# Kernel optimization log

Hardware: AMD Instinct MI355X
Metric: run time of the kernel (lower is better)

Reference implementation:

```python
import jax, jax.numpy as jnp
import numpy as np

NUM_CLASSES = 80
NUM_PRIORS = 3
STRIDES = (8, 16, 32)
ANCHORS = (((10, 13), (16, 30), (33, 23)),
           ((30, 61), (62, 45), (59, 119)),
           ((116, 90), (156, 198), (373, 326)))
PRE_TOP_K = 1000
KEEP_TOP_K = 100
IOU_THR = 0.65
SCORE_THR = 0.25
IMG = 640
CLS_OFFSET = 4096.0  # class-offset trick for batched (class-aware) NMS


def _make_priors():
    priors, strides = [], []
    for lvl, s in enumerate(STRIDES):
        fs = IMG // s
        ys, xs = np.meshgrid(np.arange(fs), np.arange(fs), indexing='ij')
        cx = (xs * s).astype(np.float32)[..., None]
        cy = (ys * s).astype(np.float32)[..., None]
        anc = np.asarray(ANCHORS[lvl], np.float32)  # [3,2]
        cx = np.broadcast_to(cx, (fs, fs, NUM_PRIORS))
        cy = np.broadcast_to(cy, (fs, fs, NUM_PRIORS))
        w = np.broadcast_to(anc[None, None, :, 0], (fs, fs, NUM_PRIORS))
        h = np.broadcast_to(anc[None, None, :, 1], (fs, fs, NUM_PRIORS))
        box = np.stack([cx - w / 2, cy - h / 2, cx + w / 2, cy + h / 2], -1).reshape(-1, 4)
        priors.append(box)
        strides.append(np.full((box.shape[0],), s, np.float32))
    return jnp.asarray(np.concatenate(priors)), jnp.asarray(np.concatenate(strides))


def setup_inputs() -> dict:
    key = jax.random.key(0)
    ks = jax.random.split(key, 9)
    shapes = {
        'cls0': (32, 240, 80, 80), 'cls1': (32, 240, 40, 40), 'cls2': (32, 240, 20, 20),
        'bbox0': (32, 12, 80, 80), 'bbox1': (32, 12, 40, 40), 'bbox2': (32, 12, 20, 20),
        'obj0': (32, 3, 80, 80), 'obj1': (32, 3, 40, 40), 'obj2': (32, 3, 20, 20),
    }
    inp = {n: jax.random.normal(k, s, dtype=jnp.float32) for (n, s), k in zip(shapes.items(), ks)}
    priors, strides = _make_priors()
    inp['priors'] = priors
    inp['strides'] = strides
    return inp


def _flatten(x, last):  # [B,C,H,W] -> [B, H*W*priors, last]
    B = x.shape[0]
    return jnp.transpose(x, (0, 2, 3, 1)).reshape(B, -1, last)


def _decode_yolov5(priors, preds, strides):
    # priors [N,4] (x1,y1,x2,y2), preds [B,N,4], strides [N]
    p = jax.nn.sigmoid(preds)
    cx = (priors[:, 0] + priors[:, 2]) * 0.5
    cy = (priors[:, 1] + priors[:, 3]) * 0.5
    w = priors[:, 2] - priors[:, 0]
    h = priors[:, 3] - priors[:, 1]
    xc = (p[..., 0] - 0.5) * 2.0 * strides + cx
    yc = (p[..., 1] - 0.5) * 2.0 * strides + cy
    wp = (p[..., 2] * 2.0) ** 2 * w
    hp = (p[..., 3] * 2.0) ** 2 * h
    return jnp.stack([xc - wp * 0.5, yc - hp * 0.5, xc + wp * 0.5, yc + hp * 0.5], -1)


def _pairwise_iou(b):  # b [K,4]
    area = (b[:, 2] - b[:, 0]) * (b[:, 3] - b[:, 1])
    lt = jnp.maximum(b[:, None, :2], b[None, :, :2])
    rb = jnp.minimum(b[:, None, 2:], b[None, :, 2:])
    wh = jnp.clip(rb - lt, 0.0)
    inter = wh[..., 0] * wh[..., 1]
    return inter / (area[:, None] + area[None, :] - inter + 1e-7)


def _nms_single(boxes, scores):
    # boxes [N,4], scores [N,C]
    flat = scores.reshape(-1)
    top_s, top_i = jax.lax.top_k(flat, PRE_TOP_K)  # sorted desc
    anchor = top_i // NUM_CLASSES
    label = top_i % NUM_CLASSES
    b = boxes[anchor]  # [K,4]
    bo = b + label.astype(boxes.dtype)[:, None] * CLS_OFFSET
    iou = _pairwise_iou(bo)
    valid = top_s > SCORE_THR
    idxs = jnp.arange(PRE_TOP_K)

    def body(i, supp):
        keep_i = jnp.logical_not(supp[i])
        return jnp.where(keep_i & (iou[i] > IOU_THR) & (idxs > i), True, supp)

    supp = jax.lax.fori_loop(0, PRE_TOP_K, body, jnp.logical_not(valid))
    keep = jnp.logical_not(supp) & valid
    k_scores = jnp.where(keep, top_s, 0.0)
    det_s, det_i = jax.lax.top_k(k_scores, KEEP_TOP_K)
    det_b = b[det_i]
    det_l = label[det_i]
    num = jnp.minimum(jnp.sum(keep.astype(jnp.int32)), KEEP_TOP_K)
    return num, det_b, det_s, det_l


def reference(cls0, cls1, cls2, bbox0, bbox1, bbox2, obj0, obj1, obj2, priors, strides):
    cls = jnp.concatenate([_flatten(c, NUM_CLASSES) for c in (cls0, cls1, cls2)], axis=1)
    scores = jax.nn.sigmoid(cls)  # [B,N,C]
    bp = jnp.concatenate([_flatten(b, 4) for b in (bbox0, bbox1, bbox2)], axis=1)
    obj = jnp.concatenate([_flatten(o, 1)[..., 0] for o in (obj0, obj1, obj2)], axis=1)
    scores = scores * jax.nn.sigmoid(obj)[..., None]
    bboxes = _decode_yolov5(priors, bp, strides)  # [B,N,4]
    num, det_b, det_s, det_l = jax.vmap(_nms_single)(bboxes, scores)
    return num, det_b, det_s, det_l
```

## Files before the change

kernel.cpp:

```cpp
#include <hip/hip_runtime.h>
#include <stdint.h>

#define NCLS 80
#define CELLS 8400
#define PRE 1000
#define KEEP 100
#define CAP 4096
#define NBINS 16384
#define NIMG 32
#define SUBS 8
#define SUBCAP 2048
#define GBINS 4096
#define COMPCAP 2048
#define T0 0.75f
#define SCREEN 1.0886f

typedef float nfloat4 __attribute__((ext_vector_type(4)));

__device__ __forceinline__ float sigm(float x) { return 1.0f / (1.0f + __expf(-x)); }

__device__ __forceinline__ void lvlinfo(int cell, int& li, int& loc, int& HW) {
  if (cell < 6400)      { li = 0; loc = cell;        HW = 6400; }
  else if (cell < 8000) { li = 1; loc = cell - 6400; HW = 1600; }
  else                  { li = 2; loc = cell - 8000; HW = 400;  }
}

__global__ __launch_bounds__(256) void k_pass1(
    const float* __restrict__ cls0, const float* __restrict__ cls1, const float* __restrict__ cls2,
    const float* __restrict__ obj0, const float* __restrict__ obj1, const float* __restrict__ obj2,
    uint32_t* __restrict__ cnt75, uint64_t* __restrict__ cand75) {
  const int b = blockIdx.y;
  const int bx = blockIdx.x;
  const int sb = bx / 6;
  const int r  = bx - sb * 6;
  const int h  = r & 1;
  const int p  = r >> 1;
  const int c0cell = (sb * 256 + threadIdx.x) * 4;
  if (c0cell >= CELLS) return;
  int li, loc, HW; lvlinfo(c0cell, li, loc, HW);
  const float* cls = li == 0 ? cls0 : (li == 1 ? cls1 : cls2);
  const float* obj = li == 0 ? obj0 : (li == 1 ? obj1 : obj2);

  float4 ov = *(const float4*)(obj + ((size_t)b * 3 + p) * HW + loc);
  float os[4] = { sigm(ov.x), sigm(ov.y), sigm(ov.z), sigm(ov.w) };

  const int sub = bx & (SUBS - 1);
  const float* cp = cls + ((size_t)b * 240 + p * 80 + h * 40) * HW + loc;

  for (int gq = 0; gq < 5; ++gq) {
    nfloat4 v[8];
#pragma unroll
    for (int u = 0; u < 8; ++u)
      v[u] = __builtin_nontemporal_load((const nfloat4*)(cp + (size_t)(gq * 8 + u) * HW));
#pragma unroll
    for (int u = 0; u < 8; ++u) {
      const int c = h * 40 + gq * 8 + u;
      float vv[4] = { v[u].x, v[u].y, v[u].z, v[u].w };
#pragma unroll
      for (int k = 0; k < 4; ++k) {
        if (vv[k] > SCREEN) {
          float s = sigm(vv[k]) * os[k];
          if (s > T0) {
            uint32_t slot = atomicAdd(&cnt75[b * SUBS + sub], 1u);
            if (slot < SUBCAP) {
              uint32_t flat = (uint32_t)(((c0cell + k) * 3 + p) * 80 + c);
              cand75[((size_t)(b * SUBS + sub)) * SUBCAP + slot] =
                  ((uint64_t)__float_as_uint(s) << 32) | (uint64_t)(0xFFFFFFFFu - flat);
            }
          }
        }
      }
    }
  }
}

__global__ __launch_bounds__(1024) void k_gather(
    const uint64_t* __restrict__ cand75, const uint32_t* __restrict__ cnt75,
    uint32_t* __restrict__ flags, uint32_t* __restrict__ histg,
    const float* __restrict__ bbox0, const float* __restrict__ bbox1, const float* __restrict__ bbox2,
    const float* __restrict__ priors, const float* __restrict__ strides,
    float* __restrict__ topS, int* __restrict__ topLab, float* __restrict__ topBox,
    uint32_t* __restrict__ nvArr) {
  __shared__ uint32_t hist[GBINS];
  __shared__ uint64_t comp[COMPCAP];
  __shared__ uint32_t seg[64];
  __shared__ uint32_t ncomp_s, cb_s;
  const int b = blockIdx.x;
  const int tid = threadIdx.x;
  uint32_t tot = 0; bool bad = false;
  for (int s = 0; s < SUBS; ++s) {
    uint32_t cc = cnt75[b * SUBS + s];
    tot += cc;
    if (cc > SUBCAP) bad = true;
  }
  if (tot < (uint32_t)PRE) bad = true;
  if (bad) {
    if (tid == 0) flags[b] = 1u;
    for (int i = tid; i < NBINS; i += 1024) histg[(size_t)b * NBINS + i] = 0;
    return;
  }

  for (int i = tid; i < GBINS; i += 1024) hist[i] = 0;
  if (tid == 0) ncomp_s = 0;
  __syncthreads();
  for (int s = 0; s < SUBS; ++s) {
    uint32_t c = cnt75[b * SUBS + s];
    const uint64_t* src = cand75 + ((size_t)(b * SUBS + s)) * SUBCAP;
    for (int i = tid; i < (int)c; i += 1024) {
      uint32_t hi = (uint32_t)(src[i] >> 32);
      uint32_t bin = (hi - 0x3F400000u) >> 10;
      if (bin > GBINS - 1) bin = GBINS - 1;
      atomicAdd(&hist[bin], 1u);
    }
  }
  __syncthreads();
  if (tid < 64) {
    uint32_t s = 0;
    for (int k = 0; k < 64; ++k) s += hist[tid * 64 + k];
    seg[tid] = s;
  }
  __syncthreads();
  if (tid == 0) {
    uint32_t acc = 0; int segi = 0;
    for (int i = 63; i >= 0; --i) {
      if (acc + seg[i] >= (uint32_t)PRE) { segi = i; break; }
      acc += seg[i];
    }
    uint32_t cb = 0;
    for (int k = 63; k >= 0; --k) {
      acc += hist[segi * 64 + k];
      if (acc >= (uint32_t)PRE) { cb = (uint32_t)(segi * 64 + k); break; }
    }
    cb_s = cb;
  }
  __syncthreads();
  const uint32_t cb = cb_s;
  for (int s = 0; s < SUBS; ++s) {
    uint32_t c = cnt75[b * SUBS + s];
    const uint64_t* src = cand75 + ((size_t)(b * SUBS + s)) * SUBCAP;
    for (int i = tid; i < (int)c; i += 1024) {
      uint64_t key = src[i];
      uint32_t hi = (uint32_t)(key >> 32);
      uint32_t bin = (hi - 0x3F400000u) >> 10;
      if (bin > GBINS - 1) bin = GBINS - 1;
      if (bin >= cb) {
        uint32_t pos = atomicAdd(&ncomp_s, 1u);
        if (pos < COMPCAP) comp[pos] = key;
      }
    }
  }
  __syncthreads();
  const uint32_t ncomp = ncomp_s;
  if (ncomp > COMPCAP) {
    if (tid == 0) flags[b] = 1u;
    for (int i = tid; i < NBINS; i += 1024) histg[(size_t)b * NBINS + i] = 0;
    return;
  }
  const int N = (ncomp <= 1024u) ? 1024 : COMPCAP;
  for (int i = tid; i < N; i += 1024) if (i >= (int)ncomp) comp[i] = 0ull;
  __syncthreads();
  for (int k = 2; k <= N; k <<= 1) {
    for (int j = k >> 1; j > 0; j >>= 1) {
      for (int i = tid; i < N; i += 1024) {
        int p = i ^ j;
        if (p > i) {
          uint64_t a = comp[i], c = comp[p];
          bool asc = (i & k) != 0;
          if (asc ? (a > c) : (a < c)) { comp[i] = c; comp[p] = a; }
        }
      }
      __syncthreads();
    }
  }
  if (tid == 0) nvArr[b] = (uint32_t)PRE;
  for (int t = tid; t < PRE; t += 1024) {
    uint64_t key = comp[t];
    float sc = __uint_as_float((uint32_t)(key >> 32));
    uint32_t flat = 0xFFFFFFFFu - (uint32_t)(key & 0xFFFFFFFFull);
    uint32_t n = flat / 80u; int lab = (int)(flat - n * 80u);
    uint32_t g = n / 3u; uint32_t p = n - g * 3u;
    int li, loc, HW; lvlinfo((int)g, li, loc, HW);
    const float* bb = li == 0 ? bbox0 : (li == 1 ? bbox1 : bbox2);
    size_t o = ((size_t)b * 12 + p * 4) * HW + loc;
    float p0 = sigm(bb[o]);
    float p1 = sigm(bb[o + (size_t)HW]);
    float p2 = sigm(bb[o + 2 * (size_t)HW]);
    float p3 = sigm(bb[o + 3 * (size_t)HW]);
    float4 pr = *(const float4*)(priors + (size_t)n * 4);
    float st = strides[n];
    float cx = (pr.x + pr.z) * 0.5f, cy = (pr.y + pr.w) * 0.5f;
    float w = pr.z - pr.x, hh = pr.w - pr.y;
    float xc = (p0 - 0.5f) * 2.0f * st + cx;
    float yc = (p1 - 0.5f) * 2.0f * st + cy;
    float wp = p2 * 2.0f; wp = wp * wp * w;
    float hp = p3 * 2.0f; hp = hp * hp * hh;
    topS[(size_t)b * PRE + t] = sc;
    topLab[(size_t)b * PRE + t] = lab;
    *(float4*)(topBox + ((size_t)b * PRE + t) * 4) =
        make_float4(xc - wp * 0.5f, yc - hp * 0.5f, xc + wp * 0.5f, yc + hp * 0.5f);
  }
}

__global__ __launch_bounds__(256) void k_hist_fb(
    const float* __restrict__ cls0, const float* __restrict__ cls1, const float* __restrict__ cls2,
    const float* __restrict__ obj0, const float* __restrict__ obj1, const float* __restrict__ obj2,
    uint32_t* __restrict__ hist, const uint32_t* __restrict__ flags,
    uint32_t* __restrict__ histDone, uint32_t* __restrict__ cutoff) {
  const int b = blockIdx.y;
  if (flags[b] == 0u) return;
  __shared__ uint32_t h[NBINS];
  __shared__ uint32_t seg[256];
  __shared__ uint32_t lastArrive;
  for (int i = threadIdx.x; i < NBINS; i += 256) h[i] = 0;
  __syncthreads();
  const int c0 = (blockIdx.x * 256 + threadIdx.x) * 4;
  if (c0 < CELLS) {
    int li, loc, HW; lvlinfo(c0, li, loc, HW);
    const float* cls = li == 0 ? cls0 : (li == 1 ? cls1 : cls2);
    const float* obj = li == 0 ? obj0 : (li == 1 ? obj1 : obj2);
    float os[3][4];
#pragma unroll
    for (int p = 0; p < 3; ++p) {
      float4 o = *(const float4*)(obj + ((size_t)b * 3 + p) * HW + loc);
      os[p][0] = sigm(o.x); os[p][1] = sigm(o.y); os[p][2] = sigm(o.z); os[p][3] = sigm(o.w);
    }
    for (int p = 0; p < 3; ++p) {
      const float* cp = cls + ((size_t)b * 240 + p * 80) * HW + loc;
      for (int c = 0; c < 80; ++c) {
        float4 v = *(const float4*)(cp + (size_t)c * HW);
        float sv[4] = { sigm(v.x) * os[p][0], sigm(v.y) * os[p][1],
                        sigm(v.z) * os[p][2], sigm(v.w) * os[p][3] };
#pragma unroll
        for (int k = 0; k < 4; ++k) {
          if (sv[k] > 0.25f) {
            uint32_t key = (__float_as_uint(sv[k]) - 0x3E800000u) >> 10;
            if (key > NBINS - 1) key = NBINS - 1;
            atomicAdd(&h[key], 1u);
          }
        }
      }
    }
  }
  __syncthreads();
  for (int i = threadIdx.x; i < NBINS; i += 256) {
    uint32_t v = h[i];
    if (v) atomicAdd(&hist[(size_t)b * NBINS + i], v);
  }
  __syncthreads();
  __threadfence();
  if (threadIdx.x == 0) lastArrive = atomicAdd(&histDone[b], 1u);
  __syncthreads();
  if (lastArrive != 8) return;
  __threadfence();
  uint32_t* hb = hist + (size_t)b * NBINS;
  uint32_t s = 0;
  for (int k = 0; k < 64; ++k) s += atomicOr(&hb[threadIdx.x * 64 + k], 0u);
  seg[threadIdx.x] = s;
  __syncthreads();
  if (threadIdx.x == 0) {
    uint32_t acc = 0; int segi = -1;
    for (int i = 255; i >= 0; --i) {
      if (acc + seg[i] >= (uint32_t)PRE) { segi = i; break; }
      acc += seg[i];
    }
    uint32_t cut = 0;
    if (segi >= 0) {
      for (int k = 63; k >= 0; --k) {
        acc += atomicOr(&hb[segi * 64 + k], 0u);
        if (acc >= (uint32_t)PRE) { cut = (uint32_t)(segi * 64 + k); break; }
      }
    }
    cutoff[b] = cut;
  }
}

__global__ __launch_bounds__(256) void k_collect_fb(
    const float* __restrict__ cls0, const float* __restrict__ cls1, const float* __restrict__ cls2,
    const float* __restrict__ obj0, const float* __restrict__ obj1, const float* __restrict__ obj2,
    const uint32_t* __restrict__ cutoff, uint32_t* __restrict__ candCount,
    uint64_t* __restrict__ cand, const uint32_t* __restrict__ flags,
    uint32_t* __restrict__ collectDone,
    const float* __restrict__ bbox0, const float* __restrict__ bbox1, const float* __restrict__ bbox2,
    const float* __restrict__ priors, const float* __restrict__ strides,
    float* __restrict__ topS, int* __restrict__ topLab, float* __restrict__ topBox,
    uint32_t* __restrict__ nvArr) {
  const int b = blockIdx.y;
  if (flags[b] == 0u) return;
  __shared__ uint64_t s[CAP];
  __shared__ uint32_t lastArrive;
  const uint32_t cut = cutoff[b];
  const int c0 = (blockIdx.x * 256 + threadIdx.x) * 4;
  if (c0 < CELLS) {
    int li, loc, HW; lvlinfo(c0, li, loc, HW);
    const float* cls = li == 0 ? cls0 : (li == 1 ? cls1 : cls2);
    const float* obj = li == 0 ? obj0 : (li == 1 ? obj1 : obj2);
    float os[3][4];
#pragma unroll
    for (int p = 0; p < 3; ++p) {
      float4 o = *(const float4*)(obj + ((size_t)b * 3 + p) * HW + loc);
      os[p][0] = sigm(o.x); os[p][1] = sigm(o.y); os[p][2] = sigm(o.z); os[p][3] = sigm(o.w);
    }
    for (int p = 0; p < 3; ++p) {
      const float* cp = cls + ((size_t)b * 240 + p * 80) * HW + loc;
      for (int c = 0; c < 80; ++c) {
        float4 v = *(const float4*)(cp + (size_t)c * HW);
        float sv[4] = { sigm(v.x) * os[p][0], sigm(v.y) * os[p][1],
                        sigm(v.z) * os[p][2], sigm(v.w) * os[p][3] };
#pragma unroll
        for (int k = 0; k < 4; ++k) {
          float sk = sv[k];
          if (sk > 0.25f) {
            uint32_t key = (__float_as_uint(sk) - 0x3E800000u) >> 10;
            if (key >= cut) {
              uint32_t pos = atomicAdd(&candCount[b], 1u);
              if (pos < CAP) {
                uint32_t flat = (uint32_t)((((c0 + k) * 3 + p) * 80) + c);
                cand[(size_t)b * CAP + pos] =
                    ((uint64_t)__float_as_uint(sk) << 32) | (uint64_t)(0xFFFFFFFFu - flat);
              }
            }
          }
        }
      }
    }
  }
  __syncthreads();
  __threadfence();
  if (threadIdx.x == 0) lastArrive = atomicAdd(&collectDone[b], 1u);
  __syncthreads();
  if (lastArrive != 8) return;
  __threadfence();
  uint32_t cnt = atomicOr(&candCount[b], 0u); if (cnt > (uint32_t)CAP) cnt = CAP;
  for (int i = threadIdx.x; i < CAP; i += 256)
    s[i] = (i < (int)cnt) ? cand[(size_t)b * CAP + i] : 0ull;
  __syncthreads();
  for (int k = 2; k <= CAP; k <<= 1) {
    for (int j = k >> 1; j > 0; j >>= 1) {
      for (int i = threadIdx.x; i < CAP; i += 256) {
        int p = i ^ j;
        if (p > i) {
          uint64_t a = s[i], c = s[p];
          bool asc = (i & k) != 0;
          if (asc ? (a > c) : (a < c)) { s[i] = c; s[p] = a; }
        }
      }
      __syncthreads();
    }
  }
  const int NV = (int)(cnt < (uint32_t)PRE ? cnt : (uint32_t)PRE);
  if (threadIdx.x == 0) nvArr[b] = (uint32_t)NV;
  for (int t = threadIdx.x; t < PRE; t += 256) {
    float sc = 0.0f; int lab = 0; float b0 = 0, b1 = 0, b2v = 0, b3 = 0;
    if (t < NV) {
      uint64_t key = s[t];
      sc = __uint_as_float((uint32_t)(key >> 32));
      uint32_t flat = 0xFFFFFFFFu - (uint32_t)(key & 0xFFFFFFFFull);
      uint32_t n = flat / 80u; lab = (int)(flat - n * 80u);
      uint32_t g = n / 3u; uint32_t p = n - g * 3u;
      int li, loc, HW; lvlinfo((int)g, li, loc, HW);
      const float* bb = li == 0 ? bbox0 : (li == 1 ? bbox1 : bbox2);
      size_t o = ((size_t)b * 12 + p * 4) * HW + loc;
      float p0 = sigm(bb[o]);
      float p1 = sigm(bb[o + (size_t)HW]);
      float p2 = sigm(bb[o + 2 * (size_t)HW]);
      float p3 = sigm(bb[o + 3 * (size_t)HW]);
      float4 pr = *(const float4*)(priors + (size_t)n * 4);
      float st = strides[n];
      float cx = (pr.x + pr.z) * 0.5f, cy = (pr.y + pr.w) * 0.5f;
      float w = pr.z - pr.x, hh = pr.w - pr.y;
      float xc = (p0 - 0.5f) * 2.0f * st + cx;
      float yc = (p1 - 0.5f) * 2.0f * st + cy;
      float wp = p2 * 2.0f; wp = wp * wp * w;
      float hp = p3 * 2.0f; hp = hp * hp * hh;
      b0 = xc - wp * 0.5f; b1 = yc - hp * 0.5f; b2v = xc + wp * 0.5f; b3 = yc + hp * 0.5f;
    }
    topS[(size_t)b * PRE + t] = sc;
    topLab[(size_t)b * PRE + t] = lab;
    *(float4*)(topBox + ((size_t)b * PRE + t) * 4) = make_float4(b0, b1, b2v, b3);
  }
}

__global__ __launch_bounds__(256) void k_iou(
    const float* __restrict__ topBox, const int* __restrict__ topLab,
    const uint32_t* __restrict__ nvArr, uint64_t* __restrict__ mask) {
  __shared__ float4 bx[PRE];
  __shared__ int lb[PRE];
  const int b = blockIdx.y;
  const int NV = (int)nvArr[b];
  for (int i = threadIdx.x; i < PRE; i += 256) {
    bx[i] = *(const float4*)(topBox + ((size_t)b * PRE + i) * 4);
    lb[i] = topLab[(size_t)b * PRE + i];
  }
  __syncthreads();
  for (int task = blockIdx.x * 256 + threadIdx.x; task < PRE * 16; task += gridDim.x * 256) {
    const int i = task >> 4, w = task & 15;
    uint64_t m = 0;
    if (i < NV) {
      const float4 a = bx[i]; const int la = lb[i];
      const float areaA = (a.z - a.x) * (a.w - a.y);
      const int j0 = w << 6;
      const int jend = (j0 + 64 < NV) ? j0 + 64 : NV;
      for (int j = (j0 > i + 1 ? j0 : i + 1); j < jend; ++j) {
        if (lb[j] != la) continue;
        const float4 c = bx[j];
        float xx1 = fmaxf(a.x, c.x), yy1 = fmaxf(a.y, c.y);
        float xx2 = fminf(a.z, c.z), yy2 = fminf(a.w, c.w);
        float iw = fmaxf(xx2 - xx1, 0.0f), ih = fmaxf(yy2 - yy1, 0.0f);
        float inter = iw * ih;
        float areaB = (c.z - c.x) * (c.w - c.y);
        float iou = inter / (areaA + areaB - inter + 1e-7f);
        if (iou > 0.65f) m |= (1ull << (j - j0));
      }
    }
    mask[((size_t)b * PRE + i) * 16 + w] = m;
  }
}

__global__ __launch_bounds__(256) void k_scan_out(
    const uint64_t* __restrict__ mask, const float* __restrict__ topS,
    const int* __restrict__ topLab, const float* __restrict__ topBox,
    const uint32_t* __restrict__ nvArr, float* __restrict__ out) {
  __shared__ uint64_t rows[PRE * 16];
  __shared__ uint64_t keepw[16];
  __shared__ uint32_t pref[17];
  const int b = blockIdx.x;
  const int NV = (int)nvArr[b];
  for (int i = threadIdx.x; i < NV * 16; i += 256) rows[i] = mask[(size_t)b * PRE * 16 + i];
  __syncthreads();
  if (threadIdx.x < 64) {
    const int lane = threadIdx.x;
    uint64_t remv = 0, kw = 0;
    for (int w0 = 0; w0 * 64 < NV; ++w0) {
      uint64_t cur = (uint64_t)__shfl((unsigned long long)remv, w0);
      const int ie = (w0 * 64 + 64 < NV) ? w0 * 64 + 64 : NV;
      int i = w0 * 64;
      for (; i + 4 <= ie; i += 4) {
        uint64_t rl[4], cw[4];
#pragma unroll
        for (int t = 0; t < 4; ++t) {
          rl[t] = rows[(i + t) * 16 + (lane & 15)];
          cw[t] = rows[(i + t) * 16 + w0];
        }
#pragma unroll
        for (int t = 0; t < 4; ++t) {
          const int bi = (i + t) & 63;
          const uint64_t keepm = ((cur >> bi) & 1ull) ? 0ull : ~0ull;
          cur |= cw[t] & keepm;
          remv |= rl[t] & keepm;
          kw |= (lane == w0) ? ((1ull << bi) & keepm) : 0ull;
        }
      }
      for (; i < ie; ++i) {
        const int bi = i & 63;
        uint64_t rl = rows[i * 16 + (lane & 15)];
        uint64_t cw = rows[i * 16 + w0];
        const uint64_t keepm = ((cur >> bi) & 1ull) ? 0ull : ~0ull;
        cur |= cw & keepm;
        remv |= rl & keepm;
        kw |= (lane == w0) ? ((1ull << bi) & keepm) : 0ull;
      }
    }
    if (lane < 16) keepw[lane] = kw;
  }
  __syncthreads();
  if (threadIdx.x == 0) {
    uint32_t a = 0;
    for (int w = 0; w < 16; ++w) { pref[w] = a; a += (uint32_t)__popcll((unsigned long long)keepw[w]); }
    pref[16] = a;
  }
  __syncthreads();
  const uint32_t total = pref[16];
  const uint32_t num = total < (uint32_t)KEEP ? total : (uint32_t)KEEP;
  float* o_num = out;
  float* o_box = out + NIMG;
  float* o_s   = out + NIMG + NIMG * KEEP * 4;
  float* o_l   = o_s + NIMG * KEEP;
  if (threadIdx.x == 0) o_num[b] = (float)num;
  const int zstart = NV < KEEP ? NV : KEEP;
  for (int sidx = zstart + threadIdx.x; sidx < KEEP; sidx += 256) {
    ((float4*)o_box)[b * KEEP + sidx] = make_float4(0, 0, 0, 0);
    o_s[b * KEEP + sidx] = 0.0f;
    o_l[b * KEEP + sidx] = 0.0f;
  }
  for (int j = threadIdx.x; j < NV; j += 256) {
    const int wi = j >> 6, bi = j & 63;
    const uint64_t kword = keepw[wi];
    const int isk = (int)((kword >> bi) & 1ull);
    const uint32_t below = pref[wi] + (uint32_t)__popcll((unsigned long long)(kword & ((1ull << bi) - 1ull)));
    const uint32_t slot = isk ? below : (total + (uint32_t)j - below);
    if (slot < (uint32_t)KEEP) {
      ((float4*)o_box)[b * KEEP + slot] = *(const float4*)(topBox + ((size_t)b * PRE + j) * 4);
      o_s[b * KEEP + slot] = isk ? topS[(size_t)b * PRE + j] : 0.0f;
      o_l[b * KEEP + slot] = (float)topLab[(size_t)b * PRE + j];
    }
  }
}

extern "C" void kernel_launch(void* const* d_in, const int* in_sizes, int n_in,
                              void* d_out, int out_size, void* d_ws, size_t ws_size,
                              hipStream_t stream) {
  (void)in_sizes; (void)n_in; (void)out_size; (void)ws_size;
  const float* cls0 = (const float*)d_in[0];
  const float* cls1 = (const float*)d_in[1];
  const float* cls2 = (const float*)d_in[2];
  const float* bbox0 = (const float*)d_in[3];
  const float* bbox1 = (const float*)d_in[4];
  const float* bbox2 = (const float*)d_in[5];
  const float* obj0 = (const float*)d_in[6];
  const float* obj1 = (const float*)d_in[7];
  const float* obj2 = (const float*)d_in[8];
  const float* priors = (const float*)d_in[9];
  const float* strides = (const float*)d_in[10];
  float* out = (float*)d_out;

  char* ws = (char*)d_ws;
  size_t off = 0;
  auto alloc = [&](size_t bytes) -> void* {
    void* p = ws + off;
    off = (off + bytes + 255) & ~(size_t)255;
    return p;
  };
  uint32_t* small       = (uint32_t*)alloc(4096);
  uint32_t* flags       = small;
  uint32_t* cnt75       = small + 32;
  uint32_t* candCount   = small + 288;
  uint32_t* cutoff      = small + 320;
  uint32_t* nvArr       = small + 352;
  uint32_t* histDone    = small + 384;
  uint32_t* collectDone = small + 416;
  uint64_t* cand75    = (uint64_t*)alloc((size_t)NIMG * SUBS * SUBCAP * 8);
  uint32_t* hist      = (uint32_t*)alloc((size_t)NIMG * NBINS * 4);
  uint64_t* cand      = (uint64_t*)alloc((size_t)NIMG * CAP * 8);
  float*    topS      = (float*)alloc((size_t)NIMG * PRE * 4);
  int*      topLab    = (int*)alloc((size_t)NIMG * PRE * 4);
  float*    topBox    = (float*)alloc((size_t)NIMG * PRE * 16);
  uint64_t* maskbuf   = (uint64_t*)alloc((size_t)NIMG * PRE * 16 * 8);

  hipError_t _e = hipMemsetAsync(small, 0, 4096, stream); (void)_e;

  k_pass1<<<dim3(54, NIMG), 256, 0, stream>>>(cls0, cls1, cls2, obj0, obj1, obj2,
                                              cnt75, cand75);
  k_gather<<<NIMG, 1024, 0, stream>>>(cand75, cnt75, flags, hist, bbox0, bbox1, bbox2,
                                      priors, strides, topS, topLab, topBox, nvArr);
  dim3 gScan(9, NIMG);
  k_hist_fb<<<gScan, 256, 0, stream>>>(cls0, cls1, cls2, obj0, obj1, obj2, hist, flags,
                                       histDone, cutoff);
  k_collect_fb<<<gScan, 256, 0, stream>>>(cls0, cls1, cls2, obj0, obj1, obj2,
                                          cutoff, candCount, cand, flags, collectDone,
                                          bbox0, bbox1, bbox2, priors, strides,
                                          topS, topLab, topBox, nvArr);
  k_iou<<<dim3(63, NIMG), 256, 0, stream>>>(topBox, topLab, nvArr, maskbuf);
  k_scan_out<<<NIMG, 256, 0, stream>>>(maskbuf, topS, topLab, topBox, nvArr, out);
}
```

Before: 346.3 us.

## Restructure pass1 as flat contiguous float4 streaming over class planes per level

The first screening pass now treats each level's class tensor as one flat contiguous array of float4s. Each block covers 2048 float4s with 8 loads per thread, issued through inline assembly. The grid grows from 54 to 247 blocks per image. Objectness is no longer preloaded per thread; it is loaded lazily only for values that pass the screen, and the channel and cell are recovered by integer division. This should give fully coalesced streaming and more memory-level parallelism, at the cost of scattered objectness reads and the loss of nontemporal hints.

```diff
diff --git a/kernel.cpp b/kernel.cpp
--- a/kernel.cpp
+++ b/kernel.cpp
@@ -15,8 +15,6 @@
 #define T0 0.75f
 #define SCREEN 1.0886f
 
-typedef float nfloat4 __attribute__((ext_vector_type(4)));
-
 __device__ __forceinline__ float sigm(float x) { return 1.0f / (1.0f + __expf(-x)); }
 
 __device__ __forceinline__ void lvlinfo(int cell, int& li, int& loc, int& HW) {
@@ -31,39 +29,65 @@
     uint32_t* __restrict__ cnt75, uint64_t* __restrict__ cand75) {
   const int b = blockIdx.y;
   const int bx = blockIdx.x;
-  const int sb = bx / 6;
-  const int r  = bx - sb * 6;
-  const int h  = r & 1;
-  const int p  = r >> 1;
-  const int c0cell = (sb * 256 + threadIdx.x) * 4;
-  if (c0cell >= CELLS) return;
-  int li, loc, HW; lvlinfo(c0cell, li, loc, HW);
-  const float* cls = li == 0 ? cls0 : (li == 1 ? cls1 : cls2);
-  const float* obj = li == 0 ? obj0 : (li == 1 ? obj1 : obj2);
-
-  float4 ov = *(const float4*)(obj + ((size_t)b * 3 + p) * HW + loc);
-  float os[4] = { sigm(ov.x), sigm(ov.y), sigm(ov.z), sigm(ov.w) };
-
+  int lvl, lb_f4, nf4, HW, nPer4, cellbase;
+  const float* clsB; const float* objB;
+  if (bx < 188)      { lvl = 0; lb_f4 = bx * 2048;         nf4 = 384000; HW = 6400; nPer4 = 1600; cellbase = 0;    clsB = cls0; objB = obj0; }
+  else if (bx < 235) { lvl = 1; lb_f4 = (bx - 188) * 2048; nf4 = 96000;  HW = 1600; nPer4 = 400;  cellbase = 6400; clsB = cls1; objB = obj1; }
+  else               { lvl = 2; lb_f4 = (bx - 235) * 2048; nf4 = 24000;  HW = 400;  nPer4 = 100;  cellbase = 8000; clsB = cls2; objB = obj2; }
+  (void)lvl;
+  const float4* plane = (const float4*)(clsB + (size_t)b * 240 * HW);
+  const float* objb = objB + (size_t)b * 3 * HW;
   const int sub = bx & (SUBS - 1);
-  const float* cp = cls + ((size_t)b * 240 + p * 80 + h * 40) * HW + loc;
-
-  for (int gq = 0; gq < 5; ++gq) {
-    nfloat4 v[8];
-#pragma unroll
-    for (int u = 0; u < 8; ++u)
-      v[u] = __builtin_nontemporal_load((const nfloat4*)(cp + (size_t)(gq * 8 + u) * HW));
-#pragma unroll
-    for (int u = 0; u < 8; ++u) {
-      const int c = h * 40 + gq * 8 + u;
-      float vv[4] = { v[u].x, v[u].y, v[u].z, v[u].w };
+  const int t0 = lb_f4 + threadIdx.x;
+
+  int idx[8]; bool val[8];
+#pragma unroll
+  for (int i = 0; i < 8; ++i) {
+    int ix = t0 + i * 256;
+    val[i] = ix < nf4;
+    idx[i] = val[i] ? ix : (nf4 - 1);
+  }
+  const float4 *a0 = plane + idx[0], *a1 = plane + idx[1], *a2 = plane + idx[2], *a3 = plane + idx[3],
+               *a4 = plane + idx[4], *a5 = plane + idx[5], *a6 = plane + idx[6], *a7 = plane + idx[7];
+  float4 v0, v1, v2, v3, v4, v5, v6, v7;
+  asm volatile(
+      "global_load_dwordx4 %0, %8, off\n\t"
+      "global_load_dwordx4 %1, %9, off\n\t"
+      "global_load_dwordx4 %2, %10, off\n\t"
+      "global_load_dwordx4 %3, %11, off\n\t"
+      "global_load_dwordx4 %4, %12, off\n\t"
+      "global_load_dwordx4 %5, %13, off\n\t"
+      "global_load_dwordx4 %6, %14, off\n\t"
+      "global_load_dwordx4 %7, %15, off\n\t"
+      "s_waitcnt vmcnt(0)"
+      : "=&v"(v0), "=&v"(v1), "=&v"(v2), "=&v"(v3),
+        "=&v"(v4), "=&v"(v5), "=&v"(v6), "=&v"(v7)
+      : "v"(a0), "v"(a1), "v"(a2), "v"(a3),
+        "v"(a4), "v"(a5), "v"(a6), "v"(a7));
+  __builtin_amdgcn_sched_barrier(0);
+
+  float4 vv8[8] = { v0, v1, v2, v3, v4, v5, v6, v7 };
+#pragma unroll
+  for (int i = 0; i < 8; ++i) {
+    if (!val[i]) continue;
+    float4 v = vv8[i];
+    float mx = fmaxf(fmaxf(v.x, v.y), fmaxf(v.z, v.w));
+    if (mx > SCREEN) {
+      const int j = idx[i];
+      const int ch = j / nPer4;
+      const int w4 = j - ch * nPer4;
+      const int p = ch / 80;
+      const int c = ch - p * 80;
+      float vv[4] = { v.x, v.y, v.z, v.w };
 #pragma unroll
       for (int k = 0; k < 4; ++k) {
         if (vv[k] > SCREEN) {
-          float s = sigm(vv[k]) * os[k];
+          float ov = objb[p * HW + w4 * 4 + k];
+          float s = sigm(vv[k]) * sigm(ov);
           if (s > T0) {
             uint32_t slot = atomicAdd(&cnt75[b * SUBS + sub], 1u);
             if (slot < SUBCAP) {
-              uint32_t flat = (uint32_t)(((c0cell + k) * 3 + p) * 80 + c);
+              uint32_t flat = (uint32_t)(((cellbase + w4 * 4 + k) * 3 + p) * 80 + c);
               cand75[((size_t)(b * SUBS + sub)) * SUBCAP + slot] =
                   ((uint64_t)__float_as_uint(s) << 32) | (uint64_t)(0xFFFFFFFFu - flat);
             }
@@ -538,8 +562,8 @@
 
   hipError_t _e = hipMemsetAsync(small, 0, 4096, stream); (void)_e;
 
-  k_pass1<<<dim3(54, NIMG), 256, 0, stream>>>(cls0, cls1, cls2, obj0, obj1, obj2,
-                                              cnt75, cand75);
+  k_pass1<<<dim3(247, NIMG), 256, 0, stream>>>(cls0, cls1, cls2, obj0, obj1, obj2,
+                                               cnt75, cand75);
   k_gather<<<NIMG, 1024, 0, stream>>>(cand75, cnt75, flags, hist, bbox0, bbox1, bbox2,
                                       priors, strides, topS, topLab, topBox, nvArr);
   dim3 gScan(9, NIMG);
```

Result: slower. 704.8 us (+103.5%).
